# Kernel optimization log

Measured on AMD Instinct MI355X. Metric: run time of the kernel, lower is better.

The kernel has to match this reference:

```python
import jax, jax.numpy as jnp
import numpy as np

MUL0, MUL1 = 64, 32          # 64x0e + 32x1e irreps_emb
D_FEAT = MUL0 + 3 * MUL1     # 160
N_T, N_Q, N_K = 64, 1024, 1024


def quat_apply(q, v):
    # q: (...,4) real-first (w,x,y,z); v: (...,3). Rotate v by q.
    w = q[..., :1]
    u = q[..., 1:]
    uv = jnp.cross(u, v)
    return v + 2.0 * (w * uv + jnp.cross(u, uv))


def split_irreps(f):
    # f: (..., 160) -> scalars (...,64), vectors (...,32,3)
    s = f[..., :MUL0]
    v = f[..., MUL0:].reshape(f.shape[:-1] + (MUL1, 3))
    return s, v


def dtp(a, b, Ws, Wv):
    # Depthwise tensor product restricted to l<=1 (SeparableFCTP analogue),
    # output irreps 1x0e + 32x1e, with SiLU activation on the scalar part.
    sa, va = split_irreps(a)
    sb, vb = split_irreps(b)
    # scalar paths: 0e*0e and 1e.1e (dot) -> 96 scalar channels
    scal = jnp.concatenate([sa * sb, jnp.einsum('...ci,...ci->...c', va, vb)], axis=-1)
    # vector paths: 0e*1e, 1e*0e, 1e x 1e (cross) -> 96 vector channels
    vec = jnp.concatenate(
        [sa[..., :MUL1, None] * vb, va * sb[..., :MUL1, None], jnp.cross(va, vb)], axis=-2)
    out_s = jax.nn.silu(scal @ Ws)                    # (...,1)
    out_v = jnp.einsum('...ci,co->...oi', vec, Wv)    # (...,32,3)
    return out_s, out_v


def get_key_features(points, key_coord, key_feat, W_key):
    # radius-style key lookup: nearest key node + smooth radial envelope + linear
    d2 = jnp.sum((points[:, None, :] - key_coord[None, :, :]) ** 2, axis=-1)  # (M, N_K)
    idx = jnp.argmin(d2, axis=-1)
    dist = jnp.sqrt(jnp.take_along_axis(d2, idx[:, None], axis=1)[:, 0])
    env = jnp.exp(-dist)[:, None]
    return (key_feat[idx] * env) @ W_key              # (M, 160)


def setup_inputs() -> dict:
    key = jax.random.key(0)
    ks = jax.random.split(key, 11)
    return {
        'T': jax.random.normal(ks[0], (N_T, 7), jnp.float32),
        'query_weight': jax.random.uniform(ks[1], (N_Q,), jnp.float32),
        'query_feature': jax.random.normal(ks[2], (N_Q, D_FEAT), jnp.float32),
        'query_coord': jax.random.normal(ks[3], (N_Q, 3), jnp.float32),
        'key_coord': jax.random.normal(ks[4], (N_K, 3), jnp.float32),
        'key_node_feature': jax.random.normal(ks[5], (N_K, D_FEAT), jnp.float32),
        'W_key': jax.random.normal(ks[6], (D_FEAT, D_FEAT), jnp.float32) / np.sqrt(D_FEAT),
        'Ws_lin': jax.random.normal(ks[7], (96, 1), jnp.float32) / np.sqrt(96.0),
        'Wv_lin': jax.random.normal(ks[8], (96, 32), jnp.float32) / np.sqrt(96.0),
        'Ws_ang': jax.random.normal(ks[9], (96, 1), jnp.float32) / np.sqrt(96.0),
        'Wv_ang': jax.random.normal(ks[10], (96, 32), jnp.float32) / np.sqrt(96.0),
    }


def reference(T, query_weight, query_feature, query_coord, key_coord,
              key_node_feature, W_key, Ws_lin, Wv_lin, Ws_ang, Wv_ang):
    n_t = T.shape[0]
    n_q = query_feature.shape[0]
    q = T[:, :4]
    q = q / jnp.linalg.norm(q, axis=-1, keepdims=True)
    X = T[:, 4:]
    # transform query coords by each pose: (N_T, N_Q, 3)
    qc_t = quat_apply(q[:, None, :], query_coord[None, :, :]) + X[:, None, :]
    # equivariant feature transform: scalars unchanged, vectors rotated
    s, v = split_irreps(query_feature)
    v_t = quat_apply(q[:, None, None, :], v[None])                    # (N_T,N_Q,32,3)
    qf_t = jnp.concatenate(
        [jnp.broadcast_to(s, (n_t,) + s.shape), v_t.reshape(n_t, n_q, 3 * MUL1)],
        axis=-1).reshape(n_t * n_q, D_FEAT)
    # key feature gather over the expanded N_T*N_Q batch
    kf = get_key_features(qc_t.reshape(-1, 3), key_coord, key_node_feature, W_key)
    # two tensor products; original drops leading scalar ([..., 1:])
    _, lin = dtp(qf_t, kf, Ws_lin, Wv_lin)
    _, ang = dtp(qf_t, kf, Ws_ang, Wv_ang)
    lin = lin.reshape(n_t, n_q, MUL1, 3).mean(axis=-2)
    ang = ang.reshape(n_t, n_q, MUL1, 3).mean(axis=-2)
    # rotate back into body frame
    qinv = q * jnp.array([1.0, -1.0, -1.0, -1.0], q.dtype)
    lin = quat_apply(qinv[:, None, :], lin)
    ang = quat_apply(qinv[:, None, :], ang)
    ang_orbital = jnp.cross(query_coord[None], lin)
    lin_vel = jnp.einsum('q,tqi->ti', query_weight, lin)
    ang_vel = jnp.einsum('q,tqi->ti', query_weight, ang_orbital + ang)
    return lin_vel, ang_vel
```

## Files before the change

### kernel.cpp

```cpp
#include <hip/hip_runtime.h>
#include <math.h>

#define NT 64
#define NQ 1024
#define NK 1024
#define WS_KW 0
#define WS_QF 131072
#define WS_WV 262144

__launch_bounds__(256)
__global__ void prep_kernel(const float* __restrict__ qfeat,
                            const float* __restrict__ keyfeat,
                            const float* __restrict__ Wkey,
                            const float* __restrict__ WvL,
                            const float* __restrict__ WvA,
                            float* __restrict__ ws,
                            float* __restrict__ out) {
  const int blk = blockIdx.x;
  const int tid = threadIdx.x;
  if (blk < 128) {
    const int g = blk * 256 + tid;
    const int r = g >> 5;
    const int c = g & 31;
    const float* kf = keyfeat + r * 160;
    const int c0 = 64 + 3 * c;
    float a0 = 0.f, a1 = 0.f, a2 = 0.f, a3 = 0.f;
#pragma unroll 4
    for (int k = 0; k < 160; ++k) {
      const float f = kf[k];
      const float* wr = Wkey + k * 160;
      a0 = fmaf(f, wr[c0 + 0], a0);
      a1 = fmaf(f, wr[c0 + 1], a1);
      a2 = fmaf(f, wr[c0 + 2], a2);
      a3 = fmaf(f, wr[c], a3);
    }
    reinterpret_cast<float4*>(ws + WS_KW)[g] = make_float4(a0, a1, a2, a3);
  } else if (blk < 256) {
    const int g = (blk - 128) * 256 + tid;
    const int p = g >> 5;
    const int c = g & 31;
    const float* q = qfeat + p * 160;
    float4 o = make_float4(q[64 + 3 * c], q[65 + 3 * c], q[66 + 3 * c], q[c]);
    reinterpret_cast<float4*>(ws + WS_QF)[c * 1024 + p] = o;
  } else {
    out[tid] = 0.f;
    if (tid < 128) out[256 + tid] = 0.f;
    if (tid < 32) {
      const int c = tid;
      float m0 = 0.f, m1 = 0.f, m2 = 0.f, m3 = 0.f, m4 = 0.f, m5 = 0.f;
      for (int o = 0; o < 32; ++o) {
        m0 += WvL[c * 32 + o];
        m1 += WvL[(32 + c) * 32 + o];
        m2 += WvL[(64 + c) * 32 + o];
        m3 += WvA[c * 32 + o];
        m4 += WvA[(32 + c) * 32 + o];
        m5 += WvA[(64 + c) * 32 + o];
      }
      float* wv = ws + WS_WV + c * 8;
      const float s = 1.0f / 32.0f;
      wv[0] = m0 * s; wv[1] = m1 * s; wv[2] = m2 * s;
      wv[3] = m3 * s; wv[4] = m4 * s; wv[5] = m5 * s;
      wv[6] = 0.f; wv[7] = 0.f;
    }
  }
}

__launch_bounds__(256)
__global__ void main_kernel(const float* __restrict__ T,
                            const float* __restrict__ qweight,
                            const float* __restrict__ qcoord,
                            const float* __restrict__ kcoord,
                            const float* __restrict__ ws,
                            float* __restrict__ out) {
  __shared__ float4 keys[1024];
  __shared__ float red[4][8];
  const int tid = threadIdx.x;
  const int t   = blockIdx.x >> 4;
  const int pg  = blockIdx.x & 15;
  const int p   = pg * 64 + (tid >> 2);
  const int sub = tid & 3;

  const float* Tt = T + t * 7;
  float qw = Tt[0], qx = Tt[1], qy = Tt[2], qz = Tt[3];
  const float Xx = Tt[4], Xy = Tt[5], Xz = Tt[6];
  const float rn = rsqrtf(qw * qw + qx * qx + qy * qy + qz * qz);
  qw *= rn; qx *= rn; qy *= rn; qz *= rn;
  const float ix = -qx, iy = -qy, iz = -qz;

  for (int j = 0; j < 4; ++j) {
    const int k = j * 256 + tid;
    keys[k] = make_float4(kcoord[k * 3 + 0], kcoord[k * 3 + 1], kcoord[k * 3 + 2], 0.f);
  }
  __syncthreads();

  const float qpx = qcoord[p * 3 + 0];
  const float qpy = qcoord[p * 3 + 1];
  const float qpz = qcoord[p * 3 + 2];

  const float uvx0 = qy * qpz - qz * qpy;
  const float uvy0 = qz * qpx - qx * qpz;
  const float uvz0 = qx * qpy - qy * qpx;
  const float qcx = qpx + 2.0f * (qw * uvx0 + (qy * uvz0 - qz * uvy0)) + Xx;
  const float qcy = qpy + 2.0f * (qw * uvy0 + (qz * uvx0 - qx * uvz0)) + Xy;
  const float qcz = qpz + 2.0f * (qw * uvz0 + (qx * uvy0 - qy * uvx0)) + Xz;

  float mv0 = 1e30f, mv1 = 1e30f;
  int mi0 = 0, mi1 = 0;
#pragma unroll 8
  for (int m = 0; m < 256; m += 2) {
    const int k0 = sub + 4 * m;
    const int k1 = k0 + 4;
    const float4 K0 = keys[k0];
    const float4 K1 = keys[k1];
    const float dx0 = qcx - K0.x, dy0 = qcy - K0.y, dz0 = qcz - K0.z;
    const float dx1 = qcx - K1.x, dy1 = qcy - K1.y, dz1 = qcz - K1.z;
    const float d0 = dx0 * dx0 + dy0 * dy0 + dz0 * dz0;
    const float d1 = dx1 * dx1 + dy1 * dy1 + dz1 * dz1;
    if (d0 < mv0) { mv0 = d0; mi0 = k0; }
    if (d1 < mv1) { mv1 = d1; mi1 = k1; }
  }
  float mv = mv0; int mi = mi0;
  if (mv1 < mv || (mv1 == mv && mi1 < mi)) { mv = mv1; mi = mi1; }
#pragma unroll
  for (int msk = 1; msk <= 2; msk <<= 1) {
    const float vo = __shfl_xor(mv, msk);
    const int   io = __shfl_xor(mi, msk);
    if (vo < mv || (vo == mv && io < mi)) { mv = vo; mi = io; }
  }
  const int minidx = mi;
  const float env = expf(-sqrtf(mv));

  const float4* kwrow = reinterpret_cast<const float4*>(ws + WS_KW) + minidx * 32;
  const float4* qfp   = reinterpret_cast<const float4*>(ws + WS_QF) + p;
  const float* wv = ws + WS_WV;
  float lx = 0.f, ly = 0.f, lz = 0.f, ax = 0.f, ay = 0.f, az = 0.f;
#pragma unroll
  for (int jj = 0; jj < 8; ++jj) {
    const int c = 4 * jj + sub;
    const float4 B = kwrow[c];
    const float4 A = qfp[c * 1024];
    const float uvx = iy * B.z - iz * B.y;
    const float uvy = iz * B.x - ix * B.z;
    const float uvz = ix * B.y - iy * B.x;
    const float bx = B.x + 2.0f * (qw * uvx + (iy * uvz - iz * uvy));
    const float by = B.y + 2.0f * (qw * uvy + (iz * uvx - ix * uvz));
    const float bz = B.z + 2.0f * (qw * uvz + (ix * uvy - iy * uvx));
    const float crx = A.y * bz - A.z * by;
    const float cry = A.z * bx - A.x * bz;
    const float crz = A.x * by - A.y * bx;
    const float* w6 = wv + c * 8;
    const float a1L = w6[0] * A.w, a2L = w6[1] * B.w, w3L = w6[2];
    const float a1A = w6[3] * A.w, a2A = w6[4] * B.w, w3A = w6[5];
    lx = fmaf(a1L, bx, fmaf(a2L, A.x, fmaf(w3L, crx, lx)));
    ly = fmaf(a1L, by, fmaf(a2L, A.y, fmaf(w3L, cry, ly)));
    lz = fmaf(a1L, bz, fmaf(a2L, A.z, fmaf(w3L, crz, lz)));
    ax = fmaf(a1A, bx, fmaf(a2A, A.x, fmaf(w3A, crx, ax)));
    ay = fmaf(a1A, by, fmaf(a2A, A.y, fmaf(w3A, cry, ay)));
    az = fmaf(a1A, bz, fmaf(a2A, A.z, fmaf(w3A, crz, az)));
  }
#pragma unroll
  for (int msk = 1; msk <= 2; msk <<= 1) {
    lx += __shfl_xor(lx, msk); ly += __shfl_xor(ly, msk); lz += __shfl_xor(lz, msk);
    ax += __shfl_xor(ax, msk); ay += __shfl_xor(ay, msk); az += __shfl_xor(az, msk);
  }
  lx *= env; ly *= env; lz *= env;
  ax *= env; ay *= env; az *= env;

  const float wp = qweight[p];
  const float ox = qpy * lz - qpz * ly;
  const float oy = qpz * lx - qpx * lz;
  const float oz = qpx * ly - qpy * lx;
  float r0 = wp * lx, r1 = wp * ly, r2 = wp * lz;
  float r3 = wp * (ox + ax), r4 = wp * (oy + ay), r5 = wp * (oz + az);

#pragma unroll
  for (int m = 32; m >= 1; m >>= 1) {
    r0 += __shfl_xor(r0, m);
    r1 += __shfl_xor(r1, m);
    r2 += __shfl_xor(r2, m);
    r3 += __shfl_xor(r3, m);
    r4 += __shfl_xor(r4, m);
    r5 += __shfl_xor(r5, m);
  }
  const int wave = tid >> 6;
  const int lane = tid & 63;
  if (lane == 0) {
    red[wave][0] = r0; red[wave][1] = r1; red[wave][2] = r2;
    red[wave][3] = r3; red[wave][4] = r4; red[wave][5] = r5;
  }
  __syncthreads();
  if (tid < 6) {
    const float s = red[0][tid] + red[1][tid] + red[2][tid] + red[3][tid];
    const int row = (tid < 3) ? (t * 3 + tid) : (192 + t * 3 + (tid - 3));
    atomicAdd(out + row, s * 0.25f);
  }
}

extern "C" void kernel_launch(void* const* d_in, const int* in_sizes, int n_in,
                              void* d_out, int out_size, void* d_ws, size_t ws_size,
                              hipStream_t stream) {
  const float* T   = (const float*)d_in[0];
  const float* qw  = (const float*)d_in[1];
  const float* qf  = (const float*)d_in[2];
  const float* qc  = (const float*)d_in[3];
  const float* kc  = (const float*)d_in[4];
  const float* kf  = (const float*)d_in[5];
  const float* Wk  = (const float*)d_in[6];
  const float* WvL = (const float*)d_in[8];
  const float* WvA = (const float*)d_in[10];
  float* out = (float*)d_out;
  float* ws  = (float*)d_ws;

  prep_kernel<<<257, 256, 0, stream>>>(qf, kf, Wk, WvL, WvA, ws, out);
  main_kernel<<<1024, 256, 0, stream>>>(T, qw, qc, kc, ws, out);
}
```

Measured before the change: 112.4 us.

## Read padded key coords via wave-uniform scalar loads and split argmin across waves

```diff
diff --git a/kernel.cpp b/kernel.cpp
--- a/kernel.cpp
+++ b/kernel.cpp
@@ -7,6 +7,7 @@
 #define WS_KW 0
 #define WS_QF 131072
 #define WS_WV 262144
+#define WS_KP 262400
 
 __launch_bounds__(256)
 __global__ void prep_kernel(const float* __restrict__ qfeat,
@@ -14,6 +15,7 @@
                             const float* __restrict__ Wkey,
                             const float* __restrict__ WvL,
                             const float* __restrict__ WvA,
+                            const float* __restrict__ kcoord,
                             float* __restrict__ ws,
                             float* __restrict__ out) {
   const int blk = blockIdx.x;
@@ -45,6 +47,12 @@
   } else {
     out[tid] = 0.f;
     if (tid < 128) out[256 + tid] = 0.f;
+    float4* kp = reinterpret_cast<float4*>(ws + WS_KP);
+#pragma unroll
+    for (int j = 0; j < 4; ++j) {
+      const int k = j * 256 + tid;
+      kp[k] = make_float4(kcoord[k * 3 + 0], kcoord[k * 3 + 1], kcoord[k * 3 + 2], 0.f);
+    }
     if (tid < 32) {
       const int c = tid;
       float m0 = 0.f, m1 = 0.f, m2 = 0.f, m3 = 0.f, m4 = 0.f, m5 = 0.f;
@@ -69,16 +77,15 @@
 __global__ void main_kernel(const float* __restrict__ T,
                             const float* __restrict__ qweight,
                             const float* __restrict__ qcoord,
-                            const float* __restrict__ kcoord,
                             const float* __restrict__ ws,
                             float* __restrict__ out) {
-  __shared__ float4 keys[1024];
+  __shared__ float2 cand[4][64];
   __shared__ float red[4][8];
-  const int tid = threadIdx.x;
-  const int t   = blockIdx.x >> 4;
-  const int pg  = blockIdx.x & 15;
-  const int p   = pg * 64 + (tid >> 2);
-  const int sub = tid & 3;
+  const int tid  = threadIdx.x;
+  const int lane = tid & 63;
+  const int wu   = __builtin_amdgcn_readfirstlane(tid >> 6);
+  const int t    = blockIdx.x >> 4;
+  const int pg   = blockIdx.x & 15;
 
   const float* Tt = T + t * 7;
   float qw = Tt[0], qx = Tt[1], qy = Tt[2], qz = Tt[3];
@@ -87,40 +94,41 @@
   qw *= rn; qx *= rn; qy *= rn; qz *= rn;
   const float ix = -qx, iy = -qy, iz = -qz;
 
-  for (int j = 0; j < 4; ++j) {
-    const int k = j * 256 + tid;
-    keys[k] = make_float4(kcoord[k * 3 + 0], kcoord[k * 3 + 1], kcoord[k * 3 + 2], 0.f);
-  }
-  __syncthreads();
-
-  const float qpx = qcoord[p * 3 + 0];
-  const float qpy = qcoord[p * 3 + 1];
-  const float qpz = qcoord[p * 3 + 2];
-
-  const float uvx0 = qy * qpz - qz * qpy;
-  const float uvy0 = qz * qpx - qx * qpz;
-  const float uvz0 = qx * qpy - qy * qpx;
-  const float qcx = qpx + 2.0f * (qw * uvx0 + (qy * uvz0 - qz * uvy0)) + Xx;
-  const float qcy = qpy + 2.0f * (qw * uvy0 + (qz * uvx0 - qx * uvz0)) + Xy;
-  const float qcz = qpz + 2.0f * (qw * uvz0 + (qx * uvy0 - qy * uvx0)) + Xz;
-
+  const int pA = pg * 64 + lane;
+  const float qax = qcoord[pA * 3 + 0];
+  const float qay = qcoord[pA * 3 + 1];
+  const float qaz = qcoord[pA * 3 + 2];
+  const float uvx0 = qy * qaz - qz * qay;
+  const float uvy0 = qz * qax - qx * qaz;
+  const float uvz0 = qx * qay - qy * qax;
+  const float qcx = qax + 2.0f * (qw * uvx0 + (qy * uvz0 - qz * uvy0)) + Xx;
+  const float qcy = qay + 2.0f * (qw * uvy0 + (qz * uvx0 - qx * uvz0)) + Xy;
+  const float qcz = qaz + 2.0f * (qw * uvz0 + (qx * uvy0 - qy * uvx0)) + Xz;
+
+  const float4* kp = reinterpret_cast<const float4*>(ws + WS_KP);
+  const int kbase = wu * 256;
   float mv0 = 1e30f, mv1 = 1e30f;
   int mi0 = 0, mi1 = 0;
 #pragma unroll 8
   for (int m = 0; m < 256; m += 2) {
-    const int k0 = sub + 4 * m;
-    const int k1 = k0 + 4;
-    const float4 K0 = keys[k0];
-    const float4 K1 = keys[k1];
+    const float4 K0 = kp[kbase + m];
+    const float4 K1 = kp[kbase + m + 1];
     const float dx0 = qcx - K0.x, dy0 = qcy - K0.y, dz0 = qcz - K0.z;
     const float dx1 = qcx - K1.x, dy1 = qcy - K1.y, dz1 = qcz - K1.z;
     const float d0 = dx0 * dx0 + dy0 * dy0 + dz0 * dz0;
     const float d1 = dx1 * dx1 + dy1 * dy1 + dz1 * dz1;
-    if (d0 < mv0) { mv0 = d0; mi0 = k0; }
-    if (d1 < mv1) { mv1 = d1; mi1 = k1; }
-  }
-  float mv = mv0; int mi = mi0;
-  if (mv1 < mv || (mv1 == mv && mi1 < mi)) { mv = mv1; mi = mi1; }
+    if (d0 < mv0) { mv0 = d0; mi0 = kbase + m; }
+    if (d1 < mv1) { mv1 = d1; mi1 = kbase + m + 1; }
+  }
+  float mvA = mv0; int miA = mi0;
+  if (mv1 < mvA || (mv1 == mvA && mi1 < miA)) { mvA = mv1; miA = mi1; }
+  cand[wu][lane] = make_float2(mvA, __int_as_float(miA));
+  __syncthreads();
+
+  const int pF  = pg * 64 + (tid >> 2);
+  const int sub = tid & 3;
+  const float2 c0 = cand[sub][tid >> 2];
+  float mv = c0.x; int mi = __float_as_int(c0.y);
 #pragma unroll
   for (int msk = 1; msk <= 2; msk <<= 1) {
     const float vo = __shfl_xor(mv, msk);
@@ -130,8 +138,12 @@
   const int minidx = mi;
   const float env = expf(-sqrtf(mv));
 
+  const float qpx = qcoord[pF * 3 + 0];
+  const float qpy = qcoord[pF * 3 + 1];
+  const float qpz = qcoord[pF * 3 + 2];
+
   const float4* kwrow = reinterpret_cast<const float4*>(ws + WS_KW) + minidx * 32;
-  const float4* qfp   = reinterpret_cast<const float4*>(ws + WS_QF) + p;
+  const float4* qfp   = reinterpret_cast<const float4*>(ws + WS_QF) + pF;
   const float* wv = ws + WS_WV;
   float lx = 0.f, ly = 0.f, lz = 0.f, ax = 0.f, ay = 0.f, az = 0.f;
 #pragma unroll
@@ -166,7 +178,7 @@
   lx *= env; ly *= env; lz *= env;
   ax *= env; ay *= env; az *= env;
 
-  const float wp = qweight[p];
+  const float wp = qweight[pF];
   const float ox = qpy * lz - qpz * ly;
   const float oy = qpz * lx - qpx * lz;
   const float oz = qpx * ly - qpy * lx;
@@ -183,8 +195,8 @@
     r5 += __shfl_xor(r5, m);
   }
   const int wave = tid >> 6;
-  const int lane = tid & 63;
-  if (lane == 0) {
+  const int lane2 = tid & 63;
+  if (lane2 == 0) {
     red[wave][0] = r0; red[wave][1] = r1; red[wave][2] = r2;
     red[wave][3] = r3; red[wave][4] = r4; red[wave][5] = r5;
   }
@@ -211,6 +223,6 @@
   float* out = (float*)d_out;
   float* ws  = (float*)d_ws;
 
-  prep_kernel<<<257, 256, 0, stream>>>(qf, kf, Wk, WvL, WvA, ws, out);
-  main_kernel<<<1024, 256, 0, stream>>>(T, qw, qc, kc, ws, out);
+  prep_kernel<<<257, 256, 0, stream>>>(qf, kf, Wk, WvL, WvA, kc, ws, out);
+  main_kernel<<<1024, 256, 0, stream>>>(T, qw, qc, ws, out);
 }
```

New measurement: 119.1 us. 5.9% more time.
